# Kernel optimization log

Measured on AMD Instinct MI355X. Metric: run time of the kernel, lower is better.

Reference implementation:

```python
import jax, jax.numpy as jnp
import numpy as np

CLIP_TANH = 10.0
M_CHECKS, N_VARS = 256, 512   # parity-check matrix shape
ROW_W = 8                     # ones per check row -> E = 256*8 = 2048 edges
BATCH = 16384


def _build_masks():
    """Tanner-graph connectivity masks, as in init_w_skipconn2even / initialize_w_v2c."""
    rng = np.random.default_rng(0)
    pcm = np.zeros((M_CHECKS, N_VARS), np.float32)
    for r in range(M_CHECKS):
        pcm[r, rng.choice(N_VARS, ROW_W, replace=False)] = 1.0
    checks, variables = np.nonzero(pcm)  # edge list, row-major order, length E
    E = checks.size
    # edge e' feeds edge e iff same variable node, different check node
    same_var = variables[:, None] == variables[None, :]
    diff_chk = checks[:, None] != checks[None, :]
    w_odd2even_mask = (same_var & diff_chk).astype(np.float32)               # [E, E]
    # variable v feeds every edge incident to it
    w_skip_mask = (np.arange(N_VARS)[:, None] == variables[None, :]).astype(np.float32)  # [N, E]
    return jnp.asarray(w_odd2even_mask), jnp.asarray(w_skip_mask), E


def setup_inputs() -> dict:
    key = jax.random.key(0)
    w_o2e_mask, w_skip_mask, E = _build_masks()
    k = jax.random.split(key, 5)
    return {
        "x": jax.random.normal(k[0], (BATCH, E), jnp.float32),          # edge messages
        "llr": jax.random.normal(k[1], (BATCH, N_VARS), jnp.float32),   # channel LLRs
        "u": jax.random.uniform(k[2], (E,), jnp.float32),               # dropout uniforms
        "odd_weights": 0.05 * jax.random.normal(k[3], (E, E), jnp.float32),
        "llr_weights": 1.0 + 0.05 * jax.random.normal(k[4], (N_VARS, E), jnp.float32),
        "dropout_logits": 10.0 * jnp.ones((E,), jnp.float32),           # 10000*LOGITS_INIT analogue (sigmoid ~ 1)
        "w_odd2even_mask": w_o2e_mask,
        "w_skipconn2even_mask": w_skip_mask,
    }


def reference(x, llr, u, odd_weights, llr_weights, dropout_logits,
              w_odd2even_mask, w_skipconn2even_mask):
    # TEST-phase forward, mask_only=False
    total_mask = w_odd2even_mask * odd_weights                        # [E, E], very sparse support
    z = (u < jax.nn.sigmoid(dropout_logits)).astype(x.dtype)          # Bernoulli gate per source edge
    mask_after_dropout = total_mask * z[:, None]                      # row-wise gating
    msg = x @ mask_after_dropout                                      # [B, E]
    skip = llr @ (w_skipconn2even_mask * llr_weights)                 # [B, E]
    odd_clamp = jnp.clip(msg + skip, -CLIP_TANH, CLIP_TANH)
    return jnp.tanh(0.5 * odd_clamp)
```

## Files before the change

kernel.cpp:

```cpp
#include <hip/hip_runtime.h>
#include <hip/hip_bf16.h>

constexpr int E     = 2048;
constexpr int NVARS = 512;
constexpr int DMAX  = 20;
constexpr int TB    = 4;
constexpr int NT    = 512;

__device__ __forceinline__ unsigned bf16hi(float f) {
    const unsigned uu = __float_as_uint(f);
    return (uu + 0x7FFFu + ((uu >> 16) & 1u)) & 0xFFFF0000u;
}
__device__ __forceinline__ unsigned cvtpk(float lo, float hi) {
    unsigned r;
    asm("v_cvt_pk_bf16_f32 %0, %1, %2" : "=v"(r) : "v"(lo), "v"(hi));
    return r;
}
__device__ __forceinline__ float bl(unsigned q) { return __uint_as_float(q << 16); }
__device__ __forceinline__ float bh(unsigned q) { return __uint_as_float(q & 0xFFFF0000u); }

typedef const __attribute__((address_space(1))) void* gas_t;
typedef __attribute__((address_space(3))) void*       las_t;

__global__ __launch_bounds__(256)
void k_vsrc(const float* __restrict__ skip_mask,
            const float* __restrict__ llr_w,
            unsigned short* __restrict__ vsrc,
            float* __restrict__ skw)
{
    const int col = blockIdx.x * 256 + threadIdx.x;
    const int v0  = blockIdx.y * (NVARS / 32);
    for (int v = v0; v < v0 + NVARS / 32; ++v) {
        const float m = skip_mask[(size_t)v * E + col];
        if (m != 0.0f) {
            vsrc[col] = (unsigned short)v;
            skw [col] = m * llr_w[(size_t)v * E + col];
        }
    }
}

__global__ __launch_bounds__(64)
void k_pervar(const unsigned short* __restrict__ vsrc,
              const float* __restrict__ skw,
              const float* __restrict__ odd_w,
              const float* __restrict__ u,
              const float* __restrict__ logits,
              uint4*  __restrict__ wtc,
              float4* __restrict__ hdr,
              int*    __restrict__ nitems)
{
    __shared__ unsigned short vs[E];
    __shared__ int deg[NVARS];
    __shared__ unsigned short mem[DMAX];
    __shared__ float zf[DMAX];
    __shared__ float sks[DMAX];

    const int v   = blockIdx.x;
    const int tid = threadIdx.x;

    for (int i = tid; i < E / 8; i += 64)
        ((uint4*)vs)[i] = ((const uint4*)vsrc)[i];
    for (int i = tid; i < NVARS; i += 64) deg[i] = 0;
    __syncthreads();
    for (int i = tid; i < E; i += 64) atomicAdd(&deg[vs[i]], 1);
    __syncthreads();

    const int dv = deg[v];

    int itot = 0, ib = 0, wb = 0;
    for (int i = tid; i < NVARS; i += 64) {
        const int d2 = deg[i];
        if (!d2) continue;
        const int dc = (d2 < DMAX) ? d2 : DMAX;
        const int ic = (dc + 3) >> 2;
        itot += ic;
        if (dv > 0 && (d2 < dv || (d2 == dv && i < v))) { ib += ic; wb += dc * ic; }
    }
    #pragma unroll
    for (int o = 32; o; o >>= 1) {
        itot += __shfl_xor(itot, o);
        ib   += __shfl_xor(ib,   o);
        wb   += __shfl_xor(wb,   o);
    }
    if (v == 0 && tid == 0) nitems[0] = itot;
    if (!dv) return;
    const int de = (dv < DMAX) ? dv : DMAX;
    const int ic = (de + 3) >> 2;

    int cnt = 0;
    for (int c = 0; c < E / 64; ++c) {
        const int e = c * 64 + tid;
        const bool m = ((int)vs[e] == v);
        const unsigned long long bal = __ballot(m);
        if (m) {
            const int pos = cnt + __popcll(bal & ((1ull << tid) - 1ull));
            if (pos < DMAX) mem[pos] = (unsigned short)e;
        }
        cnt += __popcll(bal);
    }
    __syncthreads();

    if (tid < de) {
        const int m = mem[tid];
        const float sig = 1.0f / (1.0f + __expf(-logits[m]));
        zf [tid] = (u[m] < sig) ? 1.0f : 0.0f;
        sks[tid] = skw[m];
    }
    __syncthreads();

    if (tid < ic) {
        const int o0 = tid * 4;
        float s0 = 0, s1 = 0, s2 = 0, s3 = 0;
        unsigned c0 = 0xFFFFu, c1 = 0xFFFFu, c2 = 0xFFFFu, c3 = 0xFFFFu;
        if (o0 + 0 < de) { s0 = sks[o0 + 0]; c0 = mem[o0 + 0]; }
        if (o0 + 1 < de) { s1 = sks[o0 + 1]; c1 = mem[o0 + 1]; }
        if (o0 + 2 < de) { s2 = sks[o0 + 2]; c2 = mem[o0 + 2]; }
        if (o0 + 3 < de) { s3 = sks[o0 + 3]; c3 = mem[o0 + 3]; }
        hdr[2 * (ib + tid)]     = make_float4(s0, s1, s2, s3);
        hdr[2 * (ib + tid) + 1] = make_float4(
            __uint_as_float(c0 | (c1 << 16)),
            __uint_as_float(c2 | (c3 << 16)),
            __uint_as_float((unsigned)(wb + tid * de)),
            __uint_as_float((unsigned)v | ((unsigned)de << 16)));
    }

    for (int idx = tid; idx < de * ic; idx += 64) {
        const int k = idx / de;
        const int j = idx - k * de;
        const int src = mem[j];
        unsigned g[4];
        #pragma unroll
        for (int q = 0; q < 4; ++q) {
            const int o = 4 * k + q;
            float ww = 0.0f;
            if (o < de && o != j)
                ww = odd_w[(size_t)src * E + mem[o]] * zf[j];
            g[q] = bf16hi(ww) | (unsigned)src;
        }
        wtc[wb + idx] = make_uint4(g[0], g[1], g[2], g[3]);
    }
}

__device__ __forceinline__ float th(float s) {
    float c = fminf(fmaxf(s, -10.0f), 10.0f);
    float t = __expf(c);
    return (t - 1.0f) * __builtin_amdgcn_rcpf(t + 1.0f);
}

__global__ __launch_bounds__(NT, 8)
void fused_main(const float* __restrict__ x,
                const float* __restrict__ llr,
                const uint4*  __restrict__ wtc,
                const float4* __restrict__ hdr,
                const int*    __restrict__ nitems,
                float* __restrict__ out)
{
    __shared__ float xsf[TB * E];
    __shared__ float lsf[TB * NVARS];

    const int b0   = blockIdx.x * TB;
    const int t    = threadIdx.x;
    const int wid  = t >> 6;
    const int lane = t & 63;

    {
        const float* gx = x + (size_t)b0 * E;
        #pragma unroll
        for (int rr = 0; rr < 4; ++rr) {
            const int cbase = wid * 256 + rr * 64;
            const float* gp = gx + (size_t)(cbase + lane) * 4;
            __builtin_amdgcn_global_load_lds(
                (gas_t)gp, (las_t)((char*)xsf + (size_t)cbase * 16), 16, 0, 0);
        }
        const float* gl = llr + (size_t)b0 * NVARS;
        const int cbase = wid * 64;
        const float* gp = gl + (size_t)(cbase + lane) * 4;
        __builtin_amdgcn_global_load_lds(
            (gas_t)gp, (las_t)((char*)lsf + (size_t)cbase * 16), 16, 0, 0);
    }
    __syncthreads();

    const int nit = nitems[0];

    unsigned sst[2][4][2];
    unsigned scc[2][2];

    #pragma unroll
    for (int r = 0; r < 2; ++r) {
        scc[r][0] = 0xFFFFFFFFu;
        scc[r][1] = 0xFFFFFFFFu;
        const int it = r * NT + t;
        if (it < nit) {
            const float4 ha = hdr[2 * it];
            const uint4  hb = ((const uint4*)hdr)[2 * it + 1];
            const uint4* wp = wtc + hb.z;
            const int v = hb.w & 0xFFFF;
            const int d = hb.w >> 16;

            const float lf0 = lsf[0 * NVARS + v];
            const float lf1 = lsf[1 * NVARS + v];
            const float lf2 = lsf[2 * NVARS + v];
            const float lf3 = lsf[3 * NVARS + v];

            float a[4][4];
            #pragma unroll
            for (int ii = 0; ii < 4; ++ii) {
                const float sk = (ii == 0) ? ha.x : (ii == 1) ? ha.y
                               : (ii == 2) ? ha.z : ha.w;
                a[ii][0] = sk * lf0; a[ii][1] = sk * lf1;
                a[ii][2] = sk * lf2; a[ii][3] = sk * lf3;
            }

            for (int j = 0; j < d; ++j) {
                const uint4 g = wp[j];
                const int   s = (int)(g.x & 0x7FFu);
                const float xf0 = xsf[0 * E + s];
                const float xf1 = xsf[1 * E + s];
                const float xf2 = xsf[2 * E + s];
                const float xf3 = xsf[3 * E + s];
                const float w0 = bh(g.x), w1 = bh(g.y);
                const float w2 = bh(g.z), w3 = bh(g.w);
                a[0][0] += w0 * xf0; a[0][1] += w0 * xf1;
                a[0][2] += w0 * xf2; a[0][3] += w0 * xf3;
                a[1][0] += w1 * xf0; a[1][1] += w1 * xf1;
                a[1][2] += w1 * xf2; a[1][3] += w1 * xf3;
                a[2][0] += w2 * xf0; a[2][1] += w2 * xf1;
                a[2][2] += w2 * xf2; a[2][3] += w2 * xf3;
                a[3][0] += w3 * xf0; a[3][1] += w3 * xf1;
                a[3][2] += w3 * xf2; a[3][3] += w3 * xf3;
            }

            scc[r][0] = hb.x;
            scc[r][1] = hb.y;
            #pragma unroll
            for (int ii = 0; ii < 4; ++ii) {
                sst[r][ii][0] = cvtpk(th(a[ii][0]), th(a[ii][1]));
                sst[r][ii][1] = cvtpk(th(a[ii][2]), th(a[ii][3]));
            }
        }
    }

    __syncthreads();
    unsigned* osp = (unsigned*)xsf;
    #pragma unroll
    for (int r = 0; r < 2; ++r) {
        #pragma unroll
        for (int ii = 0; ii < 4; ++ii) {
            const unsigned c = (scc[r][ii >> 1] >> ((ii & 1) * 16)) & 0xFFFFu;
            if (c != 0xFFFFu) {
                osp[0 * E + c] = sst[r][ii][0];
                osp[1 * E + c] = sst[r][ii][1];
            }
        }
    }
    __syncthreads();

    #pragma unroll
    for (int i = 0; i < 4; ++i) {
        const int p = i >> 1, hf = i & 1;
        const uint4 w4 = ((const uint4*)(osp + p * E))[t];
        float4 o;
        if (hf == 0) o = make_float4(bl(w4.x), bl(w4.y), bl(w4.z), bl(w4.w));
        else         o = make_float4(bh(w4.x), bh(w4.y), bh(w4.z), bh(w4.w));
        ((float4*)(out + (size_t)(b0 + i) * E))[t] = o;
    }
}

extern "C" void kernel_launch(void* const* d_in, const int* in_sizes, int n_in,
                              void* d_out, int out_size, void* d_ws, size_t ws_size,
                              hipStream_t stream) {
    const float* x        = (const float*)d_in[0];
    const float* llr      = (const float*)d_in[1];
    const float* u        = (const float*)d_in[2];
    const float* odd_w    = (const float*)d_in[3];
    const float* llr_w    = (const float*)d_in[4];
    const float* logits   = (const float*)d_in[5];
    const float* skip_msk = (const float*)d_in[7];
    float* out = (float*)d_out;

    const int B = in_sizes[0] / E;

    char* wsb = (char*)d_ws;
    size_t off = 0;
    uint4*          wtc  = (uint4*)(wsb + off);          off += (size_t)6144 * 16;
    float4*         hdr  = (float4*)(wsb + off);         off += (size_t)1024 * 32;
    float*          skw  = (float*)(wsb + off);          off += (size_t)E * 4;
    unsigned short* vsrc = (unsigned short*)(wsb + off); off += (size_t)E * 2;
    int*            nit  = (int*)(wsb + off);            off += 16;

    k_vsrc  <<<dim3(E / 256, 32), dim3(256), 0, stream>>>(skip_msk, llr_w, vsrc, skw);
    k_pervar<<<dim3(NVARS),       dim3(64),  0, stream>>>(vsrc, skw, odd_w, u, logits,
                                                          wtc, hdr, nit);

    fused_main<<<dim3(B / TB), dim3(NT), 0, stream>>>(x, llr, wtc, hdr, nit, out);
}
```

Measured before the change: 103.6 us.

## Double-buffer batch rows in LDS and overlap next loads with compute

Each block now handles 8 batch rows instead of 4, processed as four quarters of 2 rows each. Two LDS buffer pairs are used, so the async global_load_lds for the next quarter is issued while the current quarter is being computed and written out. The goal is to hide global load latency and reuse the per-thread header and weight-table reads across more rows. In exchange there are more barriers per block, half as many blocks in the grid, and an explicit vmcnt wait that relies on the exact count of outstanding loads.

New measurement: 130.4 us. +25.9%, slower.

```diff
diff --git a/kernel.cpp b/kernel.cpp
--- a/kernel.cpp
+++ b/kernel.cpp
@@ -4,7 +4,7 @@
 constexpr int E     = 2048;
 constexpr int NVARS = 512;
 constexpr int DMAX  = 20;
-constexpr int TB    = 4;
+constexpr int TB    = 8;
 constexpr int NT    = 512;
 
 __device__ __forceinline__ unsigned bf16hi(float f) {
@@ -147,6 +147,26 @@
     return (t - 1.0f) * __builtin_amdgcn_rcpf(t + 1.0f);
 }
 
+__device__ __forceinline__ void dma_quarter(const float* gx, const float* gl,
+                                            float* qx, float* ql,
+                                            int wid, int lane)
+{
+    #pragma unroll
+    for (int i = 0; i < 2; ++i) {
+        const int c = wid * 2 + i;
+        __builtin_amdgcn_global_load_lds(
+            (gas_t)((const char*)gx + c * 1024 + lane * 16),
+            (las_t)((char*)qx + c * 1024), 16, 0, 0);
+    }
+    #pragma unroll
+    for (int i = 0; i < 2; ++i) {
+        const int c = wid * 2 + i;
+        __builtin_amdgcn_global_load_lds(
+            (gas_t)((const char*)gl + c * 256 + lane * 4),
+            (las_t)((char*)ql + c * 256), 4, 0, 0);
+    }
+}
+
 __global__ __launch_bounds__(NT, 8)
 void fused_main(const float* __restrict__ x,
                 const float* __restrict__ llr,
@@ -155,114 +175,120 @@
                 const int*    __restrict__ nitems,
                 float* __restrict__ out)
 {
-    __shared__ float xsf[TB * E];
-    __shared__ float lsf[TB * NVARS];
+    __shared__ float qx0[2 * E];
+    __shared__ float qx1[2 * E];
+    __shared__ float ql0[2 * NVARS];
+    __shared__ float ql1[2 * NVARS];
 
     const int b0   = blockIdx.x * TB;
     const int t    = threadIdx.x;
     const int wid  = t >> 6;
     const int lane = t & 63;
-
-    {
-        const float* gx = x + (size_t)b0 * E;
+    const int nit  = nitems[0];
+
+    dma_quarter(x + (size_t)b0 * E, llr + (size_t)b0 * NVARS,
+                qx0, ql0, wid, lane);
+    asm volatile("s_waitcnt vmcnt(0)" ::: "memory");
+    __builtin_amdgcn_sched_barrier(0);
+    __builtin_amdgcn_s_barrier();
+    __builtin_amdgcn_sched_barrier(0);
+
+    #pragma unroll
+    for (int q = 0; q < 4; ++q) {
+        float* qxP = (q & 1) ? qx1 : qx0;
+        float* qlP = (q & 1) ? ql1 : ql0;
+        float* qxN = (q & 1) ? qx0 : qx1;
+        float* qlN = (q & 1) ? ql0 : ql1;
+
+        unsigned sst[2][4];
+        unsigned scc[2][2];
+
         #pragma unroll
-        for (int rr = 0; rr < 4; ++rr) {
-            const int cbase = wid * 256 + rr * 64;
-            const float* gp = gx + (size_t)(cbase + lane) * 4;
-            __builtin_amdgcn_global_load_lds(
-                (gas_t)gp, (las_t)((char*)xsf + (size_t)cbase * 16), 16, 0, 0);
-        }
-        const float* gl = llr + (size_t)b0 * NVARS;
-        const int cbase = wid * 64;
-        const float* gp = gl + (size_t)(cbase + lane) * 4;
-        __builtin_amdgcn_global_load_lds(
-            (gas_t)gp, (las_t)((char*)lsf + (size_t)cbase * 16), 16, 0, 0);
-    }
-    __syncthreads();
-
-    const int nit = nitems[0];
-
-    unsigned sst[2][4][2];
-    unsigned scc[2][2];
-
-    #pragma unroll
-    for (int r = 0; r < 2; ++r) {
-        scc[r][0] = 0xFFFFFFFFu;
-        scc[r][1] = 0xFFFFFFFFu;
-        const int it = r * NT + t;
-        if (it < nit) {
-            const float4 ha = hdr[2 * it];
-            const uint4  hb = ((const uint4*)hdr)[2 * it + 1];
-            const uint4* wp = wtc + hb.z;
-            const int v = hb.w & 0xFFFF;
-            const int d = hb.w >> 16;
-
-            const float lf0 = lsf[0 * NVARS + v];
-            const float lf1 = lsf[1 * NVARS + v];
-            const float lf2 = lsf[2 * NVARS + v];
-            const float lf3 = lsf[3 * NVARS + v];
-
-            float a[4][4];
+        for (int r = 0; r < 2; ++r) {
+            scc[r][0] = 0xFFFFFFFFu;
+            scc[r][1] = 0xFFFFFFFFu;
+            const int it = r * NT + t;
+            if (it < nit) {
+                const float4 ha = hdr[2 * it];
+                const uint4  hb = ((const uint4*)hdr)[2 * it + 1];
+                const uint4* wp = wtc + hb.z;
+                const int v = hb.w & 0xFFFF;
+                const int d = hb.w >> 16;
+
+                const float lf0 = qlP[v];
+                const float lf1 = qlP[NVARS + v];
+
+                float a[4][2];
+                #pragma unroll
+                for (int ii = 0; ii < 4; ++ii) {
+                    const float sk = (ii == 0) ? ha.x : (ii == 1) ? ha.y
+                                   : (ii == 2) ? ha.z : ha.w;
+                    a[ii][0] = sk * lf0;
+                    a[ii][1] = sk * lf1;
+                }
+
+                for (int j = 0; j < d; ++j) {
+                    const uint4 g = wp[j];
+                    const int   s = (int)(g.x & 0x7FFu);
+                    const float xf0 = qxP[s];
+                    const float xf1 = qxP[E + s];
+                    const float w0 = bh(g.x), w1 = bh(g.y);
+                    const float w2 = bh(g.z), w3 = bh(g.w);
+                    a[0][0] += w0 * xf0; a[0][1] += w0 * xf1;
+                    a[1][0] += w1 * xf0; a[1][1] += w1 * xf1;
+                    a[2][0] += w2 * xf0; a[2][1] += w2 * xf1;
+                    a[3][0] += w3 * xf0; a[3][1] += w3 * xf1;
+                }
+
+                scc[r][0] = hb.x;
+                scc[r][1] = hb.y;
+                #pragma unroll
+                for (int ii = 0; ii < 4; ++ii)
+                    sst[r][ii] = cvtpk(th(a[ii][0]), th(a[ii][1]));
+            }
+        }
+
+        asm volatile("s_waitcnt lgkmcnt(0)" ::: "memory");
+        __builtin_amdgcn_sched_barrier(0);
+        __builtin_amdgcn_s_barrier();
+        __builtin_amdgcn_sched_barrier(0);
+
+        if (q < 3) {
+            dma_quarter(x + (size_t)(b0 + 2 * (q + 1)) * E,
+                        llr + (size_t)(b0 + 2 * (q + 1)) * NVARS,
+                        qxN, qlN, wid, lane);
+            __builtin_amdgcn_sched_barrier(0);
+        }
+
+        unsigned* osp = (unsigned*)qxP;
+        #pragma unroll
+        for (int r = 0; r < 2; ++r) {
             #pragma unroll
             for (int ii = 0; ii < 4; ++ii) {
-                const float sk = (ii == 0) ? ha.x : (ii == 1) ? ha.y
-                               : (ii == 2) ? ha.z : ha.w;
-                a[ii][0] = sk * lf0; a[ii][1] = sk * lf1;
-                a[ii][2] = sk * lf2; a[ii][3] = sk * lf3;
+                const unsigned c = (scc[r][ii >> 1] >> ((ii & 1) * 16)) & 0xFFFFu;
+                if (c != 0xFFFFu) osp[c] = sst[r][ii];
             }
-
-            for (int j = 0; j < d; ++j) {
-                const uint4 g = wp[j];
-                const int   s = (int)(g.x & 0x7FFu);
-                const float xf0 = xsf[0 * E + s];
-                const float xf1 = xsf[1 * E + s];
-                const float xf2 = xsf[2 * E + s];
-                const float xf3 = xsf[3 * E + s];
-                const float w0 = bh(g.x), w1 = bh(g.y);
-                const float w2 = bh(g.z), w3 = bh(g.w);
-                a[0][0] += w0 * xf0; a[0][1] += w0 * xf1;
-                a[0][2] += w0 * xf2; a[0][3] += w0 * xf3;
-                a[1][0] += w1 * xf0; a[1][1] += w1 * xf1;
-                a[1][2] += w1 * xf2; a[1][3] += w1 * xf3;
-                a[2][0] += w2 * xf0; a[2][1] += w2 * xf1;
-                a[2][2] += w2 * xf2; a[2][3] += w2 * xf3;
-                a[3][0] += w3 * xf0; a[3][1] += w3 * xf1;
-                a[3][2] += w3 * xf2; a[3][3] += w3 * xf3;
-            }
-
-            scc[r][0] = hb.x;
-            scc[r][1] = hb.y;
-            #pragma unroll
-            for (int ii = 0; ii < 4; ++ii) {
-                sst[r][ii][0] = cvtpk(th(a[ii][0]), th(a[ii][1]));
-                sst[r][ii][1] = cvtpk(th(a[ii][2]), th(a[ii][3]));
-            }
-        }
-    }
-
-    __syncthreads();
-    unsigned* osp = (unsigned*)xsf;
-    #pragma unroll
-    for (int r = 0; r < 2; ++r) {
-        #pragma unroll
-        for (int ii = 0; ii < 4; ++ii) {
-            const unsigned c = (scc[r][ii >> 1] >> ((ii & 1) * 16)) & 0xFFFFu;
-            if (c != 0xFFFFu) {
-                osp[0 * E + c] = sst[r][ii][0];
-                osp[1 * E + c] = sst[r][ii][1];
-            }
-        }
-    }
-    __syncthreads();
-
-    #pragma unroll
-    for (int i = 0; i < 4; ++i) {
-        const int p = i >> 1, hf = i & 1;
-        const uint4 w4 = ((const uint4*)(osp + p * E))[t];
-        float4 o;
-        if (hf == 0) o = make_float4(bl(w4.x), bl(w4.y), bl(w4.z), bl(w4.w));
-        else         o = make_float4(bh(w4.x), bh(w4.y), bh(w4.z), bh(w4.w));
-        ((float4*)(out + (size_t)(b0 + i) * E))[t] = o;
+        }
+
+        asm volatile("s_waitcnt lgkmcnt(0)" ::: "memory");
+        __builtin_amdgcn_sched_barrier(0);
+        __builtin_amdgcn_s_barrier();
+        __builtin_amdgcn_sched_barrier(0);
+
+        {
+            const uint4 w4 = ((const uint4*)osp)[t];
+            ((float4*)(out + (size_t)(b0 + 2 * q) * E))[t] =
+                make_float4(bl(w4.x), bl(w4.y), bl(w4.z), bl(w4.w));
+            ((float4*)(out + (size_t)(b0 + 2 * q + 1) * E))[t] =
+                make_float4(bh(w4.x), bh(w4.y), bh(w4.z), bh(w4.w));
+        }
+
+        if (q < 3) {
+            asm volatile("s_waitcnt vmcnt(2) lgkmcnt(0)" ::: "memory");
+            __builtin_amdgcn_sched_barrier(0);
+            __builtin_amdgcn_s_barrier();
+            __builtin_amdgcn_sched_barrier(0);
+        }
     }
 }
 
```
